# Kernel tuning notes

Measured on AMD Instinct MI355X. Metric: run time of the kernel, lower is better.

## Reference

```python
import jax, jax.numpy as jnp
import numpy as np

EPS = 1e-12


def setup_inputs() -> dict:
    key = jax.random.key(0)
    k1, k2 = jax.random.split(key)
    B, P, D = 8, 4096, 2
    pred = jax.random.normal(k1, (B, P, D), dtype=jnp.float32)
    gt = jax.random.normal(k2, (B, P, D), dtype=jnp.float32)
    return {"pred": pred, "gt": gt}


def reference(pred, gt):
    # cdist(p=2): ||a||^2 + ||b||^2 - 2 a.b, clamped, sqrt  -> [B, P, P]
    p2 = jnp.sum(pred * pred, axis=-1)          # [B, P]
    g2 = jnp.sum(gt * gt, axis=-1)               # [B, P]
    cross = jnp.einsum("bnd,bmd->bnm", pred, gt)  # [B, P, P]
    d2 = p2[:, :, None] + g2[:, None, :] - 2.0 * cross
    matrix = jnp.sqrt(jnp.maximum(d2, EPS))      # [B, P_pred, P_gt]
    pred2gt_min = jnp.min(matrix, axis=1)        # min over pred index, per gt point
    gt2pred_min = jnp.min(matrix, axis=2)        # min over gt index, per pred point
    return 0.5 * (jnp.mean(pred2gt_min) + jnp.mean(gt2pred_min))
```

## Files before the change

### kernel.cpp

```cpp
#include <hip/hip_runtime.h>


#define NB    8
#define NP    4096
#define XBINS 2048
#define W     0.0048828125f
#define XMIN  -5.0f
#define INVW  204.8f
#define BSSTR (XBINS + 4)
#define WH    128

__device__ __forceinline__ int xbin(float x) {
    int i = (int)((x - XMIN) * INVW);
    return i < 0 ? 0 : (i > XBINS - 1 ? XBINS - 1 : i);
}

#define FOREACH8(M) M(0) M(1) M(2) M(3) M(4) M(5) M(6) M(7)

__global__ __launch_bounds__(256) void xSort(const float* __restrict__ pred,
                                             const float* __restrict__ gt,
                                             float2* __restrict__ P,
                                             unsigned* __restrict__ BS,
                                             float* __restrict__ out) {
    __shared__ __align__(16) float2 sp[NP];
    __shared__ unsigned cnt[XBINS];
    __shared__ unsigned waveTot[4];

    int t = threadIdx.x;
    int s = blockIdx.x;
    int b = s >> 1, side = s & 1;

    if (s == 0 && t == 0) *out = 0.0f;

    const float2* src = (const float2*)(side ? gt : pred) + (size_t)b * NP;
    float2*   dst = P  + (size_t)s * NP;
    unsigned* bs  = BS + (size_t)s * BSSTR;

#pragma unroll
    for (int i = 0; i < XBINS / 256; ++i) cnt[t + i * 256] = 0;
    __syncthreads();

    const float4* src4 = (const float4*)src;
#define DECLV(i) float4 v##i = src4[t + (i) * 256]; \
    atomicAdd(&cnt[xbin(v##i.x)], 1u); atomicAdd(&cnt[xbin(v##i.z)], 1u);
    FOREACH8(DECLV)
#undef DECLV
    __syncthreads();

    unsigned local = 0;
#pragma unroll
    for (int i = 0; i < 8; ++i) local += cnt[t * 8 + i];
    unsigned inc = local;
#pragma unroll
    for (int o = 1; o < 64; o <<= 1) {
        unsigned n = __shfl_up(inc, o, 64);
        if ((t & 63) >= o) inc += n;
    }
    if ((t & 63) == 63) waveTot[t >> 6] = inc;
    __syncthreads();
    unsigned wbase = 0;
#pragma unroll
    for (int w = 0; w < 4; ++w) if (w < (t >> 6)) wbase += waveTot[w];
    unsigned run = wbase + inc - local;
#pragma unroll
    for (int i = 0; i < 8; ++i) {
        unsigned c = cnt[t * 8 + i];
        cnt[t * 8 + i] = run;
        run += c;
    }
    __syncthreads();

    for (int i = t; i < XBINS; i += 256) bs[i] = cnt[i];
    __syncthreads();

#define SCAT(i) { \
    unsigned p0 = atomicAdd(&cnt[xbin(v##i.x)], 1u); \
    sp[p0] = (float2){v##i.x, v##i.y}; \
    unsigned p1 = atomicAdd(&cnt[xbin(v##i.z)], 1u); \
    sp[p1] = (float2){v##i.z, v##i.w}; }
    FOREACH8(SCAT)
#undef SCAT
    __syncthreads();

    const float4* sp4 = (const float4*)sp;
    float4*       dst4 = (float4*)dst;
#pragma unroll
    for (int i = 0; i < 8; ++i) dst4[t + i * 256] = sp4[t + i * 256];
}

__global__ __launch_bounds__(256) void winSearch(const float2* __restrict__ P,
                                                 const unsigned* __restrict__ BS,
                                                 float* __restrict__ out) {
    __shared__ __align__(16) float2 sp[NP];
    __shared__ __align__(16) unsigned short sbs[XBINS];

    int t     = threadIdx.x;
    int bid   = blockIdx.x;
    int qs    = bid & 15;
    int slice = bid >> 4;
    int b = qs & 7, dir = qs >> 3;

    int tgt = b * 2 + (1 - dir);
    const float2*   tp = P  + (size_t)tgt * NP;
    const unsigned* bs = BS + (size_t)tgt * BSSTR;

    const float4* tp4 = (const float4*)tp;
    float4*       sp4w = (float4*)sp;
#pragma unroll
    for (int i = 0; i < 8; ++i) sp4w[t + i * 256] = tp4[t + i * 256];
    const uint4* bs4  = (const uint4*)bs;
    uint2*       sbs2 = (uint2*)sbs;
#pragma unroll
    for (int i = 0; i < 2; ++i) {
        uint4 v = bs4[t + i * 256];
        sbs2[t + i * 256] = make_uint2(v.x | (v.y << 16), v.z | (v.w << 16));
    }

    const float2* qarr = P + (size_t)(b * 2 + dir) * NP;
    float2 q = qarr[slice * 256 + t];
    __syncthreads();

    float qx = q.x, qy = q.y;
    int r0 = (int)sbs[xbin(qx)];

    int w0 = r0 - WH;
    if (w0 < 0) w0 = 0;
    if (w0 > NP - 2 * WH) w0 = NP - 2 * WH;
    w0 &= ~1;

    float best = 3.402823466e+38f;
    const float4* spc = (const float4*)sp;
    int base = w0 >> 1;
#pragma unroll 8
    for (int k = 0; k < WH; ++k) {
        float4 v = spc[base + k];
        float dx0 = qx - v.x, dy0 = qy - v.y;
        float dx1 = qx - v.z, dy1 = qy - v.w;
        float d0 = fmaf(dx0, dx0, dy0 * dy0);
        float d1 = fmaf(dx1, dx1, dy1 * dy1);
        best = fminf(fminf(best, d0), d1);
    }

    float lbL = (w0 > 0)           ? fmaxf(qx - sp[w0].x - W, 0.0f)              : 3.0e38f;
    float lbR = (w0 + 2 * WH < NP) ? fmaxf(sp[w0 + 2 * WH - 1].x - W - qx, 0.0f) : 3.0e38f;
    bool uncert = (lbL * lbL < best) || (lbR * lbR < best);

    unsigned long long mask = __ballot(uncert);
    int lane = t & 63;
    while (mask) {
        int l = __ffsll((long long)mask) - 1;
        mask &= mask - 1;
        float qlx = __shfl(qx, l, 64);
        float qly = __shfl(qy, l, 64);
        float rb = 3.402823466e+38f;
#pragma unroll 4
        for (int i = 0; i < 32; ++i) {
            float4 v = spc[lane + i * 64];
            float dx0 = qlx - v.x, dy0 = qly - v.y;
            float dx1 = qlx - v.z, dy1 = qly - v.w;
            rb = fminf(rb, fmaf(dx0, dx0, dy0 * dy0));
            rb = fminf(rb, fmaf(dx1, dx1, dy1 * dy1));
        }
#pragma unroll
        for (int o = 32; o > 0; o >>= 1) rb = fminf(rb, __shfl_xor(rb, o, 64));
        if (lane == l) best = rb;
    }

    float v = sqrtf(fmaxf(best, 1e-12f));

#pragma unroll
    for (int o = 32; o > 0; o >>= 1) v += __shfl_down(v, o, 64);

    __shared__ float wsum[4];
    if ((t & 63) == 0) wsum[t >> 6] = v;
    __syncthreads();
    if (t == 0)
        atomicAdd(out, ((wsum[0] + wsum[1]) + (wsum[2] + wsum[3])) *
                           (0.5f / (float)(NB * NP)));
}

extern "C" void kernel_launch(void* const* d_in, const int* in_sizes, int n_in,
                              void* d_out, int out_size, void* d_ws, size_t ws_size,
                              hipStream_t stream) {
    const float* pred = (const float*)d_in[0];
    const float* gt   = (const float*)d_in[1];
    float*       out  = (float*)d_out;

    float2*   P  = (float2*)d_ws;
    unsigned* BS = (unsigned*)(P + (size_t)16 * NP);

    (void)in_sizes; (void)n_in; (void)out_size; (void)ws_size;

    xSort<<<16, 256, 0, stream>>>(pred, gt, P, BS, out);
    winSearch<<<256, 256, 0, stream>>>(P, BS, out);
}
```

Baseline: 22.63 us.

## Load only the needed x-band of targets into LDS and widen sort blocks

```diff
diff --git a/kernel.cpp b/kernel.cpp
--- a/kernel.cpp
+++ b/kernel.cpp
@@ -9,22 +9,23 @@
 #define INVW  204.8f
 #define BSSTR (XBINS + 4)
 #define WH    128
+#define BANDMAX 2048
 
 __device__ __forceinline__ int xbin(float x) {
     int i = (int)((x - XMIN) * INVW);
     return i < 0 ? 0 : (i > XBINS - 1 ? XBINS - 1 : i);
 }
 
-#define FOREACH8(M) M(0) M(1) M(2) M(3) M(4) M(5) M(6) M(7)
-
-__global__ __launch_bounds__(256) void xSort(const float* __restrict__ pred,
+#define FOREACH4(M) M(0) M(1) M(2) M(3)
+
+__global__ __launch_bounds__(512) void xSort(const float* __restrict__ pred,
                                              const float* __restrict__ gt,
                                              float2* __restrict__ P,
                                              unsigned* __restrict__ BS,
                                              float* __restrict__ out) {
     __shared__ __align__(16) float2 sp[NP];
     __shared__ unsigned cnt[XBINS];
-    __shared__ unsigned waveTot[4];
+    __shared__ unsigned waveTot[8];
 
     int t = threadIdx.x;
     int s = blockIdx.x;
@@ -37,19 +38,17 @@
     unsigned* bs  = BS + (size_t)s * BSSTR;
 
 #pragma unroll
-    for (int i = 0; i < XBINS / 256; ++i) cnt[t + i * 256] = 0;
+    for (int i = 0; i < XBINS / 512; ++i) cnt[t + i * 512] = 0;
     __syncthreads();
 
     const float4* src4 = (const float4*)src;
-#define DECLV(i) float4 v##i = src4[t + (i) * 256]; \
+#define DECLV(i) float4 v##i = src4[t + (i) * 512]; \
     atomicAdd(&cnt[xbin(v##i.x)], 1u); atomicAdd(&cnt[xbin(v##i.z)], 1u);
-    FOREACH8(DECLV)
+    FOREACH4(DECLV)
 #undef DECLV
     __syncthreads();
 
-    unsigned local = 0;
-#pragma unroll
-    for (int i = 0; i < 8; ++i) local += cnt[t * 8 + i];
+    unsigned local = cnt[t * 4] + cnt[t * 4 + 1] + cnt[t * 4 + 2] + cnt[t * 4 + 3];
     unsigned inc = local;
 #pragma unroll
     for (int o = 1; o < 64; o <<= 1) {
@@ -60,17 +59,17 @@
     __syncthreads();
     unsigned wbase = 0;
 #pragma unroll
-    for (int w = 0; w < 4; ++w) if (w < (t >> 6)) wbase += waveTot[w];
+    for (int w = 0; w < 8; ++w) if (w < (t >> 6)) wbase += waveTot[w];
     unsigned run = wbase + inc - local;
 #pragma unroll
-    for (int i = 0; i < 8; ++i) {
-        unsigned c = cnt[t * 8 + i];
-        cnt[t * 8 + i] = run;
+    for (int i = 0; i < 4; ++i) {
+        unsigned c = cnt[t * 4 + i];
+        cnt[t * 4 + i] = run;
         run += c;
     }
     __syncthreads();
 
-    for (int i = t; i < XBINS; i += 256) bs[i] = cnt[i];
+    for (int i = t; i < XBINS; i += 512) bs[i] = cnt[i];
     __syncthreads();
 
 #define SCAT(i) { \
@@ -78,21 +77,22 @@
     sp[p0] = (float2){v##i.x, v##i.y}; \
     unsigned p1 = atomicAdd(&cnt[xbin(v##i.z)], 1u); \
     sp[p1] = (float2){v##i.z, v##i.w}; }
-    FOREACH8(SCAT)
+    FOREACH4(SCAT)
 #undef SCAT
     __syncthreads();
 
     const float4* sp4 = (const float4*)sp;
     float4*       dst4 = (float4*)dst;
 #pragma unroll
-    for (int i = 0; i < 8; ++i) dst4[t + i * 256] = sp4[t + i * 256];
+    for (int i = 0; i < 4; ++i) dst4[t + i * 512] = sp4[t + i * 512];
 }
 
 __global__ __launch_bounds__(256) void winSearch(const float2* __restrict__ P,
                                                  const unsigned* __restrict__ BS,
                                                  float* __restrict__ out) {
-    __shared__ __align__(16) float2 sp[NP];
-    __shared__ __align__(16) unsigned short sbs[XBINS];
+    __shared__ __align__(16) float2 sp[BANDMAX];
+    __shared__ int redmin[4], redmax[4];
+    __shared__ float wsum[4];
 
     int t     = threadIdx.x;
     int bid   = blockIdx.x;
@@ -103,34 +103,42 @@
     int tgt = b * 2 + (1 - dir);
     const float2*   tp = P  + (size_t)tgt * NP;
     const unsigned* bs = BS + (size_t)tgt * BSSTR;
-
-    const float4* tp4 = (const float4*)tp;
-    float4*       sp4w = (float4*)sp;
-#pragma unroll
-    for (int i = 0; i < 8; ++i) sp4w[t + i * 256] = tp4[t + i * 256];
-    const uint4* bs4  = (const uint4*)bs;
-    uint2*       sbs2 = (uint2*)sbs;
-#pragma unroll
-    for (int i = 0; i < 2; ++i) {
-        uint4 v = bs4[t + i * 256];
-        sbs2[t + i * 256] = make_uint2(v.x | (v.y << 16), v.z | (v.w << 16));
-    }
+    const float4*   tp4 = (const float4*)tp;
 
     const float2* qarr = P + (size_t)(b * 2 + dir) * NP;
     float2 q = qarr[slice * 256 + t];
-    __syncthreads();
-
     float qx = q.x, qy = q.y;
-    int r0 = (int)sbs[xbin(qx)];
-
+
+    int r0 = (int)bs[xbin(qx)];
     int w0 = r0 - WH;
     if (w0 < 0) w0 = 0;
     if (w0 > NP - 2 * WH) w0 = NP - 2 * WH;
     w0 &= ~1;
 
+    int mn = w0, mx = w0;
+#pragma unroll
+    for (int o = 32; o > 0; o >>= 1) {
+        mn = min(mn, __shfl_xor(mn, o, 64));
+        mx = max(mx, __shfl_xor(mx, o, 64));
+    }
+    int lane = t & 63, wv = t >> 6;
+    if (lane == 0) { redmin[wv] = mn; redmax[wv] = mx; }
+    __syncthreads();
+    int lo = min(min(redmin[0], redmin[1]), min(redmin[2], redmin[3]));
+    int hi = max(max(redmax[0], redmax[1]), max(redmax[2], redmax[3])) + 2 * WH;
+    if (hi - lo > BANDMAX) hi = lo + BANDMAX;
+
+    int w0c = w0;
+    if (w0c > hi - 2 * WH) w0c = hi - 2 * WH;
+
+    int nf4 = (hi - lo) >> 1;
+    float4* sp4w = (float4*)sp;
+    for (int i = t; i < nf4; i += 256) sp4w[i] = tp4[(lo >> 1) + i];
+    __syncthreads();
+
     float best = 3.402823466e+38f;
     const float4* spc = (const float4*)sp;
-    int base = w0 >> 1;
+    int base = (w0c - lo) >> 1;
 #pragma unroll 8
     for (int k = 0; k < WH; ++k) {
         float4 v = spc[base + k];
@@ -141,12 +149,11 @@
         best = fminf(fminf(best, d0), d1);
     }
 
-    float lbL = (w0 > 0)           ? fmaxf(qx - sp[w0].x - W, 0.0f)              : 3.0e38f;
-    float lbR = (w0 + 2 * WH < NP) ? fmaxf(sp[w0 + 2 * WH - 1].x - W - qx, 0.0f) : 3.0e38f;
+    float lbL = (w0c > 0)           ? fmaxf(qx - sp[w0c - lo].x - W, 0.0f)                : 3.0e38f;
+    float lbR = (w0c + 2 * WH < NP) ? fmaxf(sp[w0c + 2 * WH - 1 - lo].x - W - qx, 0.0f)   : 3.0e38f;
     bool uncert = (lbL * lbL < best) || (lbR * lbR < best);
 
     unsigned long long mask = __ballot(uncert);
-    int lane = t & 63;
     while (mask) {
         int l = __ffsll((long long)mask) - 1;
         mask &= mask - 1;
@@ -155,7 +162,7 @@
         float rb = 3.402823466e+38f;
 #pragma unroll 4
         for (int i = 0; i < 32; ++i) {
-            float4 v = spc[lane + i * 64];
+            float4 v = tp4[lane + i * 64];
             float dx0 = qlx - v.x, dy0 = qly - v.y;
             float dx1 = qlx - v.z, dy1 = qly - v.w;
             rb = fminf(rb, fmaf(dx0, dx0, dy0 * dy0));
@@ -167,12 +174,9 @@
     }
 
     float v = sqrtf(fmaxf(best, 1e-12f));
-
 #pragma unroll
     for (int o = 32; o > 0; o >>= 1) v += __shfl_down(v, o, 64);
-
-    __shared__ float wsum[4];
-    if ((t & 63) == 0) wsum[t >> 6] = v;
+    if (lane == 0) wsum[wv] = v;
     __syncthreads();
     if (t == 0)
         atomicAdd(out, ((wsum[0] + wsum[1]) + (wsum[2] + wsum[3])) *
@@ -191,6 +195,6 @@
 
     (void)in_sizes; (void)n_in; (void)out_size; (void)ws_size;
 
-    xSort<<<16, 256, 0, stream>>>(pred, gt, P, BS, out);
+    xSort<<<16, 512, 0, stream>>>(pred, gt, P, BS, out);
     winSearch<<<256, 256, 0, stream>>>(P, BS, out);
 }
```

Result: slower. 26.99 us (+19.3%).

## Fuse sort and window-search kernels into one launch with flag-based inter-block sync

Applied to the files above, without the earlier changes.

```diff
diff --git a/kernel.cpp b/kernel.cpp
--- a/kernel.cpp
+++ b/kernel.cpp
@@ -9,6 +9,7 @@
 #define INVW  204.8f
 #define BSSTR (XBINS + 4)
 #define WH    128
+#define MAGIC 0x5AFE5AFEu
 
 __device__ __forceinline__ int xbin(float x) {
     int i = (int)((x - XMIN) * INVW);
@@ -17,166 +18,193 @@
 
 #define FOREACH8(M) M(0) M(1) M(2) M(3) M(4) M(5) M(6) M(7)
 
-__global__ __launch_bounds__(256) void xSort(const float* __restrict__ pred,
-                                             const float* __restrict__ gt,
-                                             float2* __restrict__ P,
-                                             unsigned* __restrict__ BS,
-                                             float* __restrict__ out) {
-    __shared__ __align__(16) float2 sp[NP];
-    __shared__ unsigned cnt[XBINS];
-    __shared__ unsigned waveTot[4];
-
-    int t = threadIdx.x;
-    int s = blockIdx.x;
-    int b = s >> 1, side = s & 1;
-
-    if (s == 0 && t == 0) *out = 0.0f;
-
-    const float2* src = (const float2*)(side ? gt : pred) + (size_t)b * NP;
-    float2*   dst = P  + (size_t)s * NP;
-    unsigned* bs  = BS + (size_t)s * BSSTR;
-
-#pragma unroll
-    for (int i = 0; i < XBINS / 256; ++i) cnt[t + i * 256] = 0;
-    __syncthreads();
-
-    const float4* src4 = (const float4*)src;
+__global__ __launch_bounds__(256) void fusedSS(const float* __restrict__ pred,
+                                               const float* __restrict__ gt,
+                                               float2* __restrict__ P,
+                                               unsigned* __restrict__ BS,
+                                               unsigned* __restrict__ flags,
+                                               unsigned* __restrict__ fc,
+                                               float* __restrict__ out) {
+    __shared__ __align__(16) unsigned char smem[41024];
+    float2* sp = (float2*)smem;
+
+    int t   = threadIdx.x;
+    int bid = blockIdx.x;
+
+    if (bid < 16) {
+        unsigned* cnt     = (unsigned*)(smem + 32768);
+        unsigned* waveTot = (unsigned*)(smem + 40960);
+
+        int s = bid, b = s >> 1, side = s & 1;
+
+        if (s == 0 && t == 0) {
+            __hip_atomic_store(out, 0.0f, __ATOMIC_RELAXED, __HIP_MEMORY_SCOPE_AGENT);
+            __hip_atomic_store(fc, 0u,   __ATOMIC_RELAXED, __HIP_MEMORY_SCOPE_AGENT);
+        }
+
+        const float2* src = (const float2*)(side ? gt : pred) + (size_t)b * NP;
+        float2*   dst = P  + (size_t)s * NP;
+        unsigned* bs  = BS + (size_t)s * BSSTR;
+
+#pragma unroll
+        for (int i = 0; i < 8; ++i) cnt[t + i * 256] = 0;
+        __syncthreads();
+
+        const float4* src4 = (const float4*)src;
 #define DECLV(i) float4 v##i = src4[t + (i) * 256]; \
-    atomicAdd(&cnt[xbin(v##i.x)], 1u); atomicAdd(&cnt[xbin(v##i.z)], 1u);
-    FOREACH8(DECLV)
+        atomicAdd(&cnt[xbin(v##i.x)], 1u); atomicAdd(&cnt[xbin(v##i.z)], 1u);
+        FOREACH8(DECLV)
 #undef DECLV
-    __syncthreads();
-
-    unsigned local = 0;
-#pragma unroll
-    for (int i = 0; i < 8; ++i) local += cnt[t * 8 + i];
-    unsigned inc = local;
-#pragma unroll
-    for (int o = 1; o < 64; o <<= 1) {
-        unsigned n = __shfl_up(inc, o, 64);
-        if ((t & 63) >= o) inc += n;
+        __syncthreads();
+
+        unsigned local = 0;
+#pragma unroll
+        for (int i = 0; i < 8; ++i) local += cnt[t * 8 + i];
+        unsigned inc = local;
+#pragma unroll
+        for (int o = 1; o < 64; o <<= 1) {
+            unsigned n = __shfl_up(inc, o, 64);
+            if ((t & 63) >= o) inc += n;
+        }
+        if ((t & 63) == 63) waveTot[t >> 6] = inc;
+        __syncthreads();
+        unsigned wbase = 0;
+#pragma unroll
+        for (int w = 0; w < 4; ++w) if (w < (t >> 6)) wbase += waveTot[w];
+        unsigned run = wbase + inc - local;
+#pragma unroll
+        for (int i = 0; i < 8; ++i) {
+            unsigned c = cnt[t * 8 + i];
+            cnt[t * 8 + i] = run;
+            run += c;
+        }
+        __syncthreads();
+
+        for (int i = t; i < XBINS; i += 256) bs[i] = cnt[i];
+        __syncthreads();
+
+#define SCAT(i) { \
+        unsigned p0 = atomicAdd(&cnt[xbin(v##i.x)], 1u); \
+        sp[p0] = (float2){v##i.x, v##i.y}; \
+        unsigned p1 = atomicAdd(&cnt[xbin(v##i.z)], 1u); \
+        sp[p1] = (float2){v##i.z, v##i.w}; }
+        FOREACH8(SCAT)
+#undef SCAT
+        __syncthreads();
+
+        const float4* sp4  = (const float4*)sp;
+        float4*       dst4 = (float4*)dst;
+#pragma unroll
+        for (int i = 0; i < 8; ++i) dst4[t + i * 256] = sp4[t + i * 256];
+
+        __syncthreads();
+        __threadfence();
+        if (t == 0)
+            __hip_atomic_store(&flags[s], MAGIC, __ATOMIC_RELEASE, __HIP_MEMORY_SCOPE_AGENT);
+
+    } else {
+        unsigned short* sbs  = (unsigned short*)(smem + 32768);
+        float*          wsum = (float*)(smem + 40960);
+
+        int sid   = bid - 16;
+        int qs    = sid & 15;
+        int slice = sid >> 4;
+        int b = qs & 7, dir = qs >> 3;
+        int qside = b * 2 + dir;
+        int tgt   = b * 2 + (1 - dir);
+
+        if (t == 0) {
+            long cap = 50000000;
+            while ((__hip_atomic_load(&flags[0],     __ATOMIC_ACQUIRE, __HIP_MEMORY_SCOPE_AGENT) != MAGIC ||
+                    __hip_atomic_load(&flags[qside], __ATOMIC_ACQUIRE, __HIP_MEMORY_SCOPE_AGENT) != MAGIC ||
+                    __hip_atomic_load(&flags[tgt],   __ATOMIC_ACQUIRE, __HIP_MEMORY_SCOPE_AGENT) != MAGIC) && --cap)
+                __builtin_amdgcn_s_sleep(1);
+            __threadfence();
+        }
+        __syncthreads();
+
+        const float2*   tp = P  + (size_t)tgt * NP;
+        const unsigned* bs = BS + (size_t)tgt * BSSTR;
+
+        const float4* tp4  = (const float4*)tp;
+        float4*       sp4w = (float4*)sp;
+#pragma unroll
+        for (int i = 0; i < 8; ++i) sp4w[t + i * 256] = tp4[t + i * 256];
+        const uint4* bs4  = (const uint4*)bs;
+        uint2*       sbs2 = (uint2*)sbs;
+#pragma unroll
+        for (int i = 0; i < 2; ++i) {
+            uint4 v = bs4[t + i * 256];
+            sbs2[t + i * 256] = make_uint2(v.x | (v.y << 16), v.z | (v.w << 16));
+        }
+
+        const float2* qarr = P + (size_t)qside * NP;
+        float2 q = qarr[slice * 256 + t];
+        __syncthreads();
+
+        float qx = q.x, qy = q.y;
+        int r0 = (int)sbs[xbin(qx)];
+
+        int w0 = r0 - WH;
+        if (w0 < 0) w0 = 0;
+        if (w0 > NP - 2 * WH) w0 = NP - 2 * WH;
+        w0 &= ~1;
+
+        float best = 3.402823466e+38f;
+        const float4* spc = (const float4*)sp;
+        int base = w0 >> 1;
+#pragma unroll 8
+        for (int k = 0; k < WH; ++k) {
+            float4 v = spc[base + k];
+            float dx0 = qx - v.x, dy0 = qy - v.y;
+            float dx1 = qx - v.z, dy1 = qy - v.w;
+            float d0 = fmaf(dx0, dx0, dy0 * dy0);
+            float d1 = fmaf(dx1, dx1, dy1 * dy1);
+            best = fminf(fminf(best, d0), d1);
+        }
+
+        float lbL = (w0 > 0)           ? fmaxf(qx - sp[w0].x - W, 0.0f)              : 3.0e38f;
+        float lbR = (w0 + 2 * WH < NP) ? fmaxf(sp[w0 + 2 * WH - 1].x - W - qx, 0.0f) : 3.0e38f;
+        bool uncert = (lbL * lbL < best) || (lbR * lbR < best);
+
+        unsigned long long mask = __ballot(uncert);
+        int lane = t & 63;
+        while (mask) {
+            int l = __ffsll((long long)mask) - 1;
+            mask &= mask - 1;
+            float qlx = __shfl(qx, l, 64);
+            float qly = __shfl(qy, l, 64);
+            float rb = 3.402823466e+38f;
+#pragma unroll 4
+            for (int i = 0; i < 32; ++i) {
+                float4 v = spc[lane + i * 64];
+                float dx0 = qlx - v.x, dy0 = qly - v.y;
+                float dx1 = qlx - v.z, dy1 = qly - v.w;
+                rb = fminf(rb, fmaf(dx0, dx0, dy0 * dy0));
+                rb = fminf(rb, fmaf(dx1, dx1, dy1 * dy1));
+            }
+#pragma unroll
+            for (int o = 32; o > 0; o >>= 1) rb = fminf(rb, __shfl_xor(rb, o, 64));
+            if (lane == l) best = rb;
+        }
+
+        float v = sqrtf(fmaxf(best, 1e-12f));
+#pragma unroll
+        for (int o = 32; o > 0; o >>= 1) v += __shfl_down(v, o, 64);
+        if (lane == 0) wsum[t >> 6] = v;
+        __syncthreads();
+        if (t == 0) {
+            atomicAdd(out, ((wsum[0] + wsum[1]) + (wsum[2] + wsum[3])) *
+                               (0.5f / (float)(NB * NP)));
+            unsigned old = atomicAdd(fc, 1u);
+            if (old == 255u) {
+#pragma unroll
+                for (int j = 0; j < 16; ++j)
+                    __hip_atomic_store(&flags[j], 0u, __ATOMIC_RELAXED, __HIP_MEMORY_SCOPE_AGENT);
+                __hip_atomic_store(fc, 0u, __ATOMIC_RELAXED, __HIP_MEMORY_SCOPE_AGENT);
+            }
+        }
     }
-    if ((t & 63) == 63) waveTot[t >> 6] = inc;
-    __syncthreads();
-    unsigned wbase = 0;
-#pragma unroll
-    for (int w = 0; w < 4; ++w) if (w < (t >> 6)) wbase += waveTot[w];
-    unsigned run = wbase + inc - local;
-#pragma unroll
-    for (int i = 0; i < 8; ++i) {
-        unsigned c = cnt[t * 8 + i];
-        cnt[t * 8 + i] = run;
-        run += c;
-    }
-    __syncthreads();
-
-    for (int i = t; i < XBINS; i += 256) bs[i] = cnt[i];
-    __syncthreads();
-
-#define SCAT(i) { \
-    unsigned p0 = atomicAdd(&cnt[xbin(v##i.x)], 1u); \
-    sp[p0] = (float2){v##i.x, v##i.y}; \
-    unsigned p1 = atomicAdd(&cnt[xbin(v##i.z)], 1u); \
-    sp[p1] = (float2){v##i.z, v##i.w}; }
-    FOREACH8(SCAT)
-#undef SCAT
-    __syncthreads();
-
-    const float4* sp4 = (const float4*)sp;
-    float4*       dst4 = (float4*)dst;
-#pragma unroll
-    for (int i = 0; i < 8; ++i) dst4[t + i * 256] = sp4[t + i * 256];
-}
-
-__global__ __launch_bounds__(256) void winSearch(const float2* __restrict__ P,
-                                                 const unsigned* __restrict__ BS,
-                                                 float* __restrict__ out) {
-    __shared__ __align__(16) float2 sp[NP];
-    __shared__ __align__(16) unsigned short sbs[XBINS];
-
-    int t     = threadIdx.x;
-    int bid   = blockIdx.x;
-    int qs    = bid & 15;
-    int slice = bid >> 4;
-    int b = qs & 7, dir = qs >> 3;
-
-    int tgt = b * 2 + (1 - dir);
-    const float2*   tp = P  + (size_t)tgt * NP;
-    const unsigned* bs = BS + (size_t)tgt * BSSTR;
-
-    const float4* tp4 = (const float4*)tp;
-    float4*       sp4w = (float4*)sp;
-#pragma unroll
-    for (int i = 0; i < 8; ++i) sp4w[t + i * 256] = tp4[t + i * 256];
-    const uint4* bs4  = (const uint4*)bs;
-    uint2*       sbs2 = (uint2*)sbs;
-#pragma unroll
-    for (int i = 0; i < 2; ++i) {
-        uint4 v = bs4[t + i * 256];
-        sbs2[t + i * 256] = make_uint2(v.x | (v.y << 16), v.z | (v.w << 16));
-    }
-
-    const float2* qarr = P + (size_t)(b * 2 + dir) * NP;
-    float2 q = qarr[slice * 256 + t];
-    __syncthreads();
-
-    float qx = q.x, qy = q.y;
-    int r0 = (int)sbs[xbin(qx)];
-
-    int w0 = r0 - WH;
-    if (w0 < 0) w0 = 0;
-    if (w0 > NP - 2 * WH) w0 = NP - 2 * WH;
-    w0 &= ~1;
-
-    float best = 3.402823466e+38f;
-    const float4* spc = (const float4*)sp;
-    int base = w0 >> 1;
-#pragma unroll 8
-    for (int k = 0; k < WH; ++k) {
-        float4 v = spc[base + k];
-        float dx0 = qx - v.x, dy0 = qy - v.y;
-        float dx1 = qx - v.z, dy1 = qy - v.w;
-        float d0 = fmaf(dx0, dx0, dy0 * dy0);
-        float d1 = fmaf(dx1, dx1, dy1 * dy1);
-        best = fminf(fminf(best, d0), d1);
-    }
-
-    float lbL = (w0 > 0)           ? fmaxf(qx - sp[w0].x - W, 0.0f)              : 3.0e38f;
-    float lbR = (w0 + 2 * WH < NP) ? fmaxf(sp[w0 + 2 * WH - 1].x - W - qx, 0.0f) : 3.0e38f;
-    bool uncert = (lbL * lbL < best) || (lbR * lbR < best);
-
-    unsigned long long mask = __ballot(uncert);
-    int lane = t & 63;
-    while (mask) {
-        int l = __ffsll((long long)mask) - 1;
-        mask &= mask - 1;
-        float qlx = __shfl(qx, l, 64);
-        float qly = __shfl(qy, l, 64);
-        float rb = 3.402823466e+38f;
-#pragma unroll 4
-        for (int i = 0; i < 32; ++i) {
-            float4 v = spc[lane + i * 64];
-            float dx0 = qlx - v.x, dy0 = qly - v.y;
-            float dx1 = qlx - v.z, dy1 = qly - v.w;
-            rb = fminf(rb, fmaf(dx0, dx0, dy0 * dy0));
-            rb = fminf(rb, fmaf(dx1, dx1, dy1 * dy1));
-        }
-#pragma unroll
-        for (int o = 32; o > 0; o >>= 1) rb = fminf(rb, __shfl_xor(rb, o, 64));
-        if (lane == l) best = rb;
-    }
-
-    float v = sqrtf(fmaxf(best, 1e-12f));
-
-#pragma unroll
-    for (int o = 32; o > 0; o >>= 1) v += __shfl_down(v, o, 64);
-
-    __shared__ float wsum[4];
-    if ((t & 63) == 0) wsum[t >> 6] = v;
-    __syncthreads();
-    if (t == 0)
-        atomicAdd(out, ((wsum[0] + wsum[1]) + (wsum[2] + wsum[3])) *
-                           (0.5f / (float)(NB * NP)));
 }
 
 extern "C" void kernel_launch(void* const* d_in, const int* in_sizes, int n_in,
@@ -186,11 +214,12 @@
     const float* gt   = (const float*)d_in[1];
     float*       out  = (float*)d_out;
 
-    float2*   P  = (float2*)d_ws;
-    unsigned* BS = (unsigned*)(P + (size_t)16 * NP);
+    float2*   P     = (float2*)d_ws;
+    unsigned* BS    = (unsigned*)(P + (size_t)16 * NP);
+    unsigned* flags = BS + (size_t)16 * BSSTR;
+    unsigned* fc    = flags + 16;
 
     (void)in_sizes; (void)n_in; (void)out_size; (void)ws_size;
 
-    xSort<<<16, 256, 0, stream>>>(pred, gt, P, BS, out);
-    winSearch<<<256, 256, 0, stream>>>(P, BS, out);
+    fusedSS<<<272, 256, 0, stream>>>(pred, gt, P, BS, flags, fc, out);
 }
```

New measurement: 65.55 us. 190% more time.

## Read sorted targets directly from global memory in window search, drop LDS staging

Applied to the files above, without the earlier changes.

```diff
diff --git a/kernel.cpp b/kernel.cpp
--- a/kernel.cpp
+++ b/kernel.cpp
@@ -91,9 +91,6 @@
 __global__ __launch_bounds__(256) void winSearch(const float2* __restrict__ P,
                                                  const unsigned* __restrict__ BS,
                                                  float* __restrict__ out) {
-    __shared__ __align__(16) float2 sp[NP];
-    __shared__ __align__(16) unsigned short sbs[XBINS];
-
     int t     = threadIdx.x;
     int bid   = blockIdx.x;
     int qs    = bid & 15;
@@ -101,39 +98,27 @@
     int b = qs & 7, dir = qs >> 3;
 
     int tgt = b * 2 + (1 - dir);
-    const float2*   tp = P  + (size_t)tgt * NP;
-    const unsigned* bs = BS + (size_t)tgt * BSSTR;
-
-    const float4* tp4 = (const float4*)tp;
-    float4*       sp4w = (float4*)sp;
-#pragma unroll
-    for (int i = 0; i < 8; ++i) sp4w[t + i * 256] = tp4[t + i * 256];
-    const uint4* bs4  = (const uint4*)bs;
-    uint2*       sbs2 = (uint2*)sbs;
-#pragma unroll
-    for (int i = 0; i < 2; ++i) {
-        uint4 v = bs4[t + i * 256];
-        sbs2[t + i * 256] = make_uint2(v.x | (v.y << 16), v.z | (v.w << 16));
-    }
+    const float4*   tp4 = (const float4*)(P + (size_t)tgt * NP);
+    const unsigned* bs  = BS + (size_t)tgt * BSSTR;
 
     const float2* qarr = P + (size_t)(b * 2 + dir) * NP;
     float2 q = qarr[slice * 256 + t];
-    __syncthreads();
+    float qx = q.x, qy = q.y;
 
-    float qx = q.x, qy = q.y;
-    int r0 = (int)sbs[xbin(qx)];
-
+    int r0 = (int)bs[xbin(qx)];
     int w0 = r0 - WH;
     if (w0 < 0) w0 = 0;
     if (w0 > NP - 2 * WH) w0 = NP - 2 * WH;
     w0 &= ~1;
+    int base = w0 >> 1;
 
     float best = 3.402823466e+38f;
-    const float4* spc = (const float4*)sp;
-    int base = w0 >> 1;
+    float firstx = 0.0f, lastx = 0.0f;
 #pragma unroll 8
     for (int k = 0; k < WH; ++k) {
-        float4 v = spc[base + k];
+        float4 v = tp4[base + k];
+        if (k == 0)      firstx = v.x;
+        if (k == WH - 1) lastx  = v.z;
         float dx0 = qx - v.x, dy0 = qy - v.y;
         float dx1 = qx - v.z, dy1 = qy - v.w;
         float d0 = fmaf(dx0, dx0, dy0 * dy0);
@@ -141,8 +126,8 @@
         best = fminf(fminf(best, d0), d1);
     }
 
-    float lbL = (w0 > 0)           ? fmaxf(qx - sp[w0].x - W, 0.0f)              : 3.0e38f;
-    float lbR = (w0 + 2 * WH < NP) ? fmaxf(sp[w0 + 2 * WH - 1].x - W - qx, 0.0f) : 3.0e38f;
+    float lbL = (w0 > 0)           ? fmaxf(qx - firstx - W, 0.0f) : 3.0e38f;
+    float lbR = (w0 + 2 * WH < NP) ? fmaxf(lastx - W - qx, 0.0f)  : 3.0e38f;
     bool uncert = (lbL * lbL < best) || (lbR * lbR < best);
 
     unsigned long long mask = __ballot(uncert);
@@ -155,7 +140,7 @@
         float rb = 3.402823466e+38f;
 #pragma unroll 4
         for (int i = 0; i < 32; ++i) {
-            float4 v = spc[lane + i * 64];
+            float4 v = tp4[lane + i * 64];
             float dx0 = qlx - v.x, dy0 = qly - v.y;
             float dx1 = qlx - v.z, dy1 = qly - v.w;
             rb = fminf(rb, fmaf(dx0, dx0, dy0 * dy0));
@@ -167,16 +152,10 @@
     }
 
     float v = sqrtf(fmaxf(best, 1e-12f));
-
 #pragma unroll
     for (int o = 32; o > 0; o >>= 1) v += __shfl_down(v, o, 64);
-
-    __shared__ float wsum[4];
-    if ((t & 63) == 0) wsum[t >> 6] = v;
-    __syncthreads();
-    if (t == 0)
-        atomicAdd(out, ((wsum[0] + wsum[1]) + (wsum[2] + wsum[3])) *
-                           (0.5f / (float)(NB * NP)));
+    if (lane == 0)
+        atomicAdd(out, v * (0.5f / (float)(NB * NP)));
 }
 
 extern "C" void kernel_launch(void* const* d_in, const int* in_sizes, int n_in,
```

New measurement: 33.60 us. 1.48x slower.
